# Kernel tuning notes

Hardware: AMD Instinct MI355X
Metric: run time of the kernel (lower is better)

The kernel has to match this reference:

```python
import jax, jax.numpy as jnp
import numpy as np

LEVELS = [(64, 64), (32, 32), (16, 16), (8, 8)]  # (H, W) per feature level
B, C, NH, NL, NP, NLAYERS, FFN = 8, 256, 8, 4, 4, 6, 1024
Q = sum(h * w for h, w in LEVELS)  # 5440
DH = C // NH


def setup_inputs() -> dict:
    key = jax.random.key(0)
    ks = iter(jax.random.split(key, 40))
    def rn(shape, s=0.02):
        return jax.random.normal(next(ks), shape, dtype=jnp.float32) * s
    return {
        'src_flat': jax.random.normal(next(ks), (B, Q, C), dtype=jnp.float32),
        'pos_flat': jax.random.normal(next(ks), (B, Q, C), dtype=jnp.float32) * 0.1,
        'level_embed': rn((NL, C), 0.1),
        'W_samp': rn((NLAYERS, C, NH * NL * NP * 2)),
        'b_samp': rn((NLAYERS, NH * NL * NP * 2), 0.1),
        'W_attn': rn((NLAYERS, C, NH * NL * NP)),
        'b_attn': rn((NLAYERS, NH * NL * NP), 0.1),
        'W_val': rn((NLAYERS, C, C)),
        'b_val': jnp.zeros((NLAYERS, C), jnp.float32),
        'W_out': rn((NLAYERS, C, C)),
        'b_out': jnp.zeros((NLAYERS, C), jnp.float32),
        'g1': jnp.ones((NLAYERS, C), jnp.float32),
        'b1': jnp.zeros((NLAYERS, C), jnp.float32),
        'W_fc1': rn((NLAYERS, C, FFN)),
        'b_fc1': jnp.zeros((NLAYERS, FFN), jnp.float32),
        'W_fc2': rn((NLAYERS, FFN, C)),
        'b_fc2': jnp.zeros((NLAYERS, C), jnp.float32),
        'g2': jnp.ones((NLAYERS, C), jnp.float32),
        'b2': jnp.zeros((NLAYERS, C), jnp.float32),
    }


def layer_norm(x, g, b):
    m = x.mean(-1, keepdims=True)
    v = ((x - m) ** 2).mean(-1, keepdims=True)
    return (x - m) * jax.lax.rsqrt(v + 1e-5) * g + b


def get_reference_points():
    # valid_ratios are all ones (masks are all-False), so ref pts are identical per level dim
    pts = []
    for (h, w) in LEVELS:
        ry = (jnp.arange(h, dtype=jnp.float32) + 0.5) / h
        rx = (jnp.arange(w, dtype=jnp.float32) + 0.5) / w
        yy, xx = jnp.meshgrid(ry, rx, indexing='ij')
        pts.append(jnp.stack([xx.ravel(), yy.ravel()], -1))
    return jnp.concatenate(pts, 0)  # [Q, 2] in (x, y)


def ms_deform_attn(query, src, ref_pts, Ws, bs, Wa, ba, Wv, bv, Wo, bo):
    value = (src @ Wv + bv).reshape(B, Q, NH, DH)
    off = (query @ Ws + bs).reshape(B, Q, NH, NL, NP, 2)
    aw = jax.nn.softmax((query @ Wa + ba).reshape(B, Q, NH, NL * NP), axis=-1)
    aw = aw.reshape(B, Q, NH, NL, NP).transpose(0, 2, 1, 3, 4)  # [B,NH,Q,NL,NP]
    normalizer = jnp.array([[w, h] for (h, w) in LEVELS], jnp.float32)  # (x, y) per level
    loc = ref_pts[None, :, None, None, None, :] + off / normalizer[None, None, None, :, None, :]
    out = jnp.zeros((B, NH, Q, DH), jnp.float32)
    start = 0
    for l, (h, w) in enumerate(LEVELS):
        v_l = value[:, start:start + h * w].transpose(0, 2, 1, 3)  # [B,NH,HW,DH]
        start += h * w
        loc_l = loc[:, :, :, l]  # [B,Q,NH,NP,2]
        x = loc_l[..., 0] * w - 0.5  # grid_sample align_corners=False pixel coords
        y = loc_l[..., 1] * h - 0.5
        x0 = jnp.floor(x)
        y0 = jnp.floor(y)
        fx = x - x0
        fy = y - y0
        sampled = jnp.zeros((B, NH, Q, NP, DH), jnp.float32)
        for dy, dx in ((0, 0), (0, 1), (1, 0), (1, 1)):
            cy = y0 + dy
            cx = x0 + dx
            wgt = (fy if dy else 1.0 - fy) * (fx if dx else 1.0 - fx)
            valid = (cy >= 0) & (cy < h) & (cx >= 0) & (cx < w)  # zero padding
            wgt = jnp.where(valid, wgt, 0.0)
            idx = (jnp.clip(cy, 0, h - 1) * w + jnp.clip(cx, 0, w - 1)).astype(jnp.int32)
            idx = idx.transpose(0, 2, 1, 3).reshape(B, NH, Q * NP)
            g = jnp.take_along_axis(v_l, idx[..., None], axis=2).reshape(B, NH, Q, NP, DH)
            sampled = sampled + g * wgt.transpose(0, 2, 1, 3)[..., None]
        out = out + (sampled * aw[:, :, :, l, :, None]).sum(3)
    out = out.transpose(0, 2, 1, 3).reshape(B, Q, C)
    return out @ Wo + bo


def reference(src_flat, pos_flat, level_embed, W_samp, b_samp, W_attn, b_attn, W_val, b_val, W_out, b_out, g1, b1, W_fc1, b_fc1, W_fc2, b_fc2, g2, b2):
    counts = np.array([h * w for h, w in LEVELS])
    lvl_emb = jnp.repeat(level_embed, counts, axis=0, total_repeat_length=Q)  # [Q,C]
    pos = pos_flat + lvl_emb[None]
    ref = get_reference_points()
    out = src_flat
    for i in range(NLAYERS):
        q = out + pos
        attn = ms_deform_attn(q, out, ref, W_samp[i], b_samp[i], W_attn[i], b_attn[i], W_val[i], b_val[i], W_out[i], b_out[i])
        out = layer_norm(out + attn, g1[i], b1[i])
        hid = jax.nn.relu(out @ W_fc1[i] + b_fc1[i]) @ W_fc2[i] + b_fc2[i]
        out = layer_norm(out + hid, g2[i], b2[i])
    return out
```

## Files before the change

### kernel.cpp

```cpp
#include <hip/hip_runtime.h>
#include <hip/hip_bf16.h>

#define NB 8
#define NC 256
#define NH_ 8
#define NLAYERS_ 6
#define FFN_ 1024
#define Q_ 5440
#define DH_ 32
#define M_ (NB*Q_)
#define MCH (M_/4)

typedef __attribute__((ext_vector_type(8))) short bf16x8;
typedef __attribute__((ext_vector_type(4))) short bf16x4;
typedef __attribute__((ext_vector_type(4))) float f32x4;
typedef __attribute__((ext_vector_type(4))) int i32x4;
typedef __attribute__((ext_vector_type(4))) unsigned int u32x4;
typedef unsigned int u32;

__device__ __forceinline__ unsigned short f2bf(float f) {
  unsigned int u = __float_as_uint(f);
  u += 0x7fffu + ((u >> 16) & 1u);
  return (unsigned short)(u >> 16);
}
__device__ __forceinline__ float bf2f(unsigned short s) {
  return __uint_as_float(((unsigned int)s) << 16);
}
__device__ __forceinline__ void gl16(const unsigned short* g, unsigned short* l) {
  __builtin_amdgcn_global_load_lds((const __attribute__((address_space(1))) u32*)(g),
                                   (__attribute__((address_space(3))) u32*)(l), 16, 0, 0);
}

__global__ void transpose_w2_k(const float* __restrict__ W, unsigned short* __restrict__ Wt,
                               int L, int Kd, int Nd, int NdTot, int nOff) {
  size_t total = (size_t)L * Nd * Kd;
  for (size_t i = (size_t)blockIdx.x * blockDim.x + threadIdx.x; i < total;
       i += (size_t)gridDim.x * blockDim.x) {
    int k = (int)(i % Kd);
    size_t r = i / Kd;
    int n = (int)(r % Nd);
    int l = (int)(r / Nd);
    Wt[((size_t)l * NdTot + nOff + n) * Kd + k] = f2bf(W[((size_t)l * Kd + k) * Nd + n]);
  }
}

__global__ void bias_cat_k(const float* __restrict__ bs, const float* __restrict__ ba,
                           float* __restrict__ bsa) {
  int i = blockIdx.x * blockDim.x + threadIdx.x;
  if (i >= NLAYERS_ * 384) return;
  int l = i / 384, n = i % 384;
  bsa[i] = (n < 256) ? bs[l * 256 + n] : ba[l * 128 + (n - 256)];
}

__global__ __launch_bounds__(256)
void pre_k(const float* __restrict__ src, const float* __restrict__ pf,
           const float* __restrict__ le, unsigned short* __restrict__ xb,
           unsigned short* __restrict__ pe, unsigned short* __restrict__ qb) {
  int row = blockIdx.x * 4 + (threadIdx.x >> 6);
  int lane = threadIdx.x & 63;
  size_t base = (size_t)row * NC + lane * 4;
  int q = row % Q_;
  int lvl = q < 4096 ? 0 : (q < 5120 ? 1 : (q < 5376 ? 2 : 3));
  f32x4 xv = *(const f32x4*)(src + base);
  f32x4 pv = *(const f32x4*)(pf + base) + *(const f32x4*)(le + lvl * NC + lane * 4);
  f32x4 qv = xv + pv;
  bf16x4 xo, po, qo;
#pragma unroll
  for (int j = 0; j < 4; ++j) {
    xo[j] = (short)f2bf(xv[j]); po[j] = (short)f2bf(pv[j]); qo[j] = (short)f2bf(qv[j]);
  }
  *(bf16x4*)(xb + base) = xo;
  *(bf16x4*)(pe + base) = po;
  *(bf16x4*)(qb + base) = qo;
}

__device__ __forceinline__ int swz(int r, int sl) { return sl ^ (r & 3) ^ ((r >> 2) & 3); }

template <bool RELU>
__global__ __launch_bounds__(256)
void gemm_k(const unsigned short* __restrict__ X, const unsigned short* __restrict__ Wt,
            const float* __restrict__ bias, unsigned short* __restrict__ Y,
            int Kdim, int Ndim) {
  __shared__ unsigned short Alds[2][128 * 32];
  __shared__ unsigned short Blds[2][128 * 32];
  const int t = threadIdx.x;
  const int n0 = blockIdx.x * 128;
  const int m0 = blockIdx.y * 128;
  const int wave = t >> 6, lane = t & 63;
  const int wr = wave >> 1, wc = wave & 1;
  const int lr = lane & 15, lk = lane >> 4;
  const int r0 = t >> 2, sl0 = t & 3;
  const int r1 = (256 + t) >> 2;
  const int gs0 = swz(r0, sl0);
  const int gs1 = swz(r1, sl0);
  const unsigned short* xp0 = X + (size_t)(m0 + r0) * Kdim + gs0 * 8;
  const unsigned short* wp0 = Wt + (size_t)(n0 + r0) * Kdim + gs0 * 8;
  const unsigned short* xp1 = X + (size_t)(m0 + r1) * Kdim + gs1 * 8;
  const unsigned short* wp1 = Wt + (size_t)(n0 + r1) * Kdim + gs1 * 8;

  f32x4 acc[4][4];
#pragma unroll
  for (int i = 0; i < 4; ++i)
#pragma unroll
    for (int j = 0; j < 4; ++j)
#pragma unroll
      for (int e = 0; e < 4; ++e) acc[i][j][e] = 0.f;

  auto stage = [&](int buf, int kt) {
    gl16(xp0 + kt, Alds[buf] + t * 8);
    gl16(wp0 + kt, Blds[buf] + t * 8);
    gl16(xp1 + kt, Alds[buf] + (256 + t) * 8);
    gl16(wp1 + kt, Blds[buf] + (256 + t) * 8);
  };

  stage(0, 0);
  __syncthreads();
  const int nt = Kdim >> 5;
  int cur = 0;
  for (int ti = 0; ti < nt; ++ti) {
    if (ti + 1 < nt) stage(cur ^ 1, (ti + 1) << 5);
    bf16x8 ar[4], br[4];
#pragma unroll
    for (int fi = 0; fi < 4; ++fi) {
      int r = wr * 64 + fi * 16 + lr;
      ar[fi] = *(const bf16x8*)&Alds[cur][r * 32 + swz(r, lk) * 8];
    }
#pragma unroll
    for (int fj = 0; fj < 4; ++fj) {
      int r = wc * 64 + fj * 16 + lr;
      br[fj] = *(const bf16x8*)&Blds[cur][r * 32 + swz(r, lk) * 8];
    }
#pragma unroll
    for (int fi = 0; fi < 4; ++fi)
#pragma unroll
      for (int fj = 0; fj < 4; ++fj)
        acc[fi][fj] = __builtin_amdgcn_mfma_f32_16x16x32_bf16(ar[fi], br[fj], acc[fi][fj], 0, 0, 0);
    __syncthreads();
    cur ^= 1;
  }

  const int orow = m0 + wr * 64;
  const int ocol = n0 + wc * 64;
#pragma unroll
  for (int fi = 0; fi < 4; ++fi)
#pragma unroll
    for (int fj = 0; fj < 4; ++fj) {
      int col = ocol + fj * 16 + lr;
      float bv = bias[col];
#pragma unroll
      for (int rr = 0; rr < 4; ++rr) {
        int row = orow + fi * 16 + lk * 4 + rr;
        float v = acc[fi][fj][rr] + bv;
        if constexpr (RELU) v = fmaxf(v, 0.f);
        Y[(size_t)row * Ndim + col] = f2bf(v);
      }
    }
}

__global__ __launch_bounds__(256)
void samp_k(const unsigned short* __restrict__ value, const unsigned short* __restrict__ sa,
            unsigned short* __restrict__ attn_feat) {
  __shared__ float lw[4][128][4];
  __shared__ int   la[4][128][4];
  const int wid = threadIdx.x >> 6, lane = threadIdx.x & 63;
  const int bq = blockIdx.x * 4 + wid;
  const int q = bq % Q_;
  const int b = bq / Q_;

  int lvl = q < 4096 ? 0 : (q < 5120 ? 1 : (q < 5376 ? 2 : 3));
  int qrem = q - (lvl == 0 ? 0 : lvl == 1 ? 4096 : lvl == 2 ? 5120 : 5376);
  int wlog = 6 - lvl;
  float inv = __uint_as_float((unsigned)(127 - wlog) << 23);
  float refx = ((qrem & ((1 << wlog) - 1)) + 0.5f) * inv;
  float refy = ((qrem >> wlog) + 0.5f) * inv;
  const unsigned short* sa_bq = sa + (size_t)bq * 384;

  const int h_s = lane >> 3;
  const int s0 = (lane & 7) * 2;
  unsigned lg01 = *(const unsigned*)&sa_bq[256 + h_s * 16 + s0];
  float lg0 = bf2f((unsigned short)(lg01 & 0xffff));
  float lg1 = bf2f((unsigned short)(lg01 >> 16));
  float mx = fmaxf(lg0, lg1);
  mx = fmaxf(mx, __shfl_xor(mx, 1));
  mx = fmaxf(mx, __shfl_xor(mx, 2));
  mx = fmaxf(mx, __shfl_xor(mx, 4));
  float e0 = __expf(lg0 - mx), e1 = __expf(lg1 - mx);
  float sm = e0 + e1;
  sm += __shfl_xor(sm, 1);
  sm += __shfl_xor(sm, 2);
  sm += __shfl_xor(sm, 4);
  float rs = 1.0f / sm;

#pragma unroll
  for (int j = 0; j < 2; ++j) {
    int s = s0 + j;
    float aw = (j ? e1 : e0) * rs;
    unsigned oxy = *(const unsigned*)&sa_bq[h_s * 32 + s * 2];
    float ox = bf2f((unsigned short)(oxy & 0xffff));
    float oy = bf2f((unsigned short)(oxy >> 16));
    int sl = s >> 2;
    int swl = 6 - sl;
    int sw = 1 << swl;
    int sstart = (sl == 0) ? 0 : (sl == 1) ? 4096 : (sl == 2) ? 5120 : 5376;
    float x = fmaf(refx, (float)sw, ox) - 0.5f;
    float y = fmaf(refy, (float)sw, oy) - 0.5f;
    float x0f = floorf(x), y0f = floorf(y);
    float fx = x - x0f, fy = y - y0f;
    int x0 = (int)x0f, y0 = (int)y0f;
    int rowbase = b * Q_ + sstart;
    f32x4 wv; i32x4 av;
#pragma unroll
    for (int c = 0; c < 4; ++c) {
      int dy = c >> 1, dx = c & 1;
      int cy = y0 + dy, cx = x0 + dx;
      float wgt = (dy ? fy : 1.f - fy) * (dx ? fx : 1.f - fx);
      bool valid = (cy >= 0) & (cy < sw) & (cx >= 0) & (cx < sw);
      wgt = valid ? wgt : 0.f;
      int ccy = min(max(cy, 0), sw - 1);
      int ccx = min(max(cx, 0), sw - 1);
      wv[c] = wgt * aw;
      av[c] = ((rowbase + (ccy << swl) + ccx) * NH_ + h_s) * DH_;
    }
    int idx = s * 8 + (h_s ^ (s & 7));
    *(f32x4*)&lw[wid][idx][0] = wv;
    *(i32x4*)&la[wid][idx][0] = av;
  }
  __syncthreads();

  const int h = lane >> 3;
  const int half = (lane >> 2) & 1;
  const int quad = lane & 3;
  const unsigned short* vq = value + quad * 8;
  f32x4 accA = {0.f, 0.f, 0.f, 0.f}, accB = {0.f, 0.f, 0.f, 0.f};
#pragma unroll
  for (int i = 0; i < 8; ++i) {
    int s = half * 8 + i;
    int idx = s * 8 + (h ^ (s & 7));
    f32x4 wv = *(const f32x4*)&lw[wid][idx][0];
    i32x4 av = *(const i32x4*)&la[wid][idx][0];
#pragma unroll
    for (int c = 0; c < 4; ++c) {
      u32x4 g = *(const u32x4*)(vq + av[c]);
      f32x4 v0, v1;
      v0[0] = __uint_as_float(g[0] << 16); v0[1] = __uint_as_float(g[0] & 0xffff0000u);
      v0[2] = __uint_as_float(g[1] << 16); v0[3] = __uint_as_float(g[1] & 0xffff0000u);
      v1[0] = __uint_as_float(g[2] << 16); v1[1] = __uint_as_float(g[2] & 0xffff0000u);
      v1[2] = __uint_as_float(g[3] << 16); v1[3] = __uint_as_float(g[3] & 0xffff0000u);
      float wcc = wv[c];
      accA += v0 * wcc;
      accB += v1 * wcc;
    }
  }
#pragma unroll
  for (int j = 0; j < 4; ++j) {
    accA[j] += __shfl_xor(accA[j], 4);
    accB[j] += __shfl_xor(accB[j], 4);
  }
  if (half == 0) {
    bf16x8 ov;
    ov[0] = (short)f2bf(accA[0]); ov[1] = (short)f2bf(accA[1]);
    ov[2] = (short)f2bf(accA[2]); ov[3] = (short)f2bf(accA[3]);
    ov[4] = (short)f2bf(accB[0]); ov[5] = (short)f2bf(accB[1]);
    ov[6] = (short)f2bf(accB[2]); ov[7] = (short)f2bf(accB[3]);
    *(bf16x8*)(attn_feat + (size_t)bq * NC + h * DH_ + quad * 8) = ov;
  }
}

__device__ __forceinline__ f32x4 ln_core(f32x4 xv, const float* g, const float* bta, int lane) {
  float ssum = xv[0] + xv[1] + xv[2] + xv[3];
#pragma unroll
  for (int o = 1; o <= 32; o <<= 1) ssum += __shfl_xor(ssum, o);
  float mean = ssum * (1.0f / NC);
  f32x4 cv = xv - mean;
  float s2 = cv[0] * cv[0] + cv[1] * cv[1] + cv[2] * cv[2] + cv[3] * cv[3];
#pragma unroll
  for (int o = 1; o <= 32; o <<= 1) s2 += __shfl_xor(s2, o);
  float rstd = rsqrtf(s2 * (1.0f / NC) + 1e-5f);
  f32x4 gv = *(const f32x4*)(g + lane * 4);
  f32x4 bv = *(const f32x4*)(bta + lane * 4);
  return cv * rstd * gv + bv;
}
__device__ __forceinline__ f32x4 ldbf4(const unsigned short* p) {
  bf16x4 v = *(const bf16x4*)p;
  f32x4 r;
#pragma unroll
  for (int j = 0; j < 4; ++j) r[j] = bf2f((unsigned short)v[j]);
  return r;
}
__device__ __forceinline__ void stbf4(unsigned short* p, f32x4 v) {
  bf16x4 o;
#pragma unroll
  for (int j = 0; j < 4; ++j) o[j] = (short)f2bf(v[j]);
  *(bf16x4*)p = o;
}

__global__ __launch_bounds__(256)
void ln_mid_k(const unsigned short* __restrict__ xb, const unsigned short* __restrict__ delta,
              const float* __restrict__ g, const float* __restrict__ bta,
              unsigned short* __restrict__ xm) {
  int row = blockIdx.x * 4 + (threadIdx.x >> 6);
  int lane = threadIdx.x & 63;
  size_t base = (size_t)row * NC + lane * 4;
  f32x4 xv = ldbf4(xb + base) + ldbf4(delta + base);
  f32x4 ov = ln_core(xv, g, bta, lane);
  stbf4(xm + base, ov);
}

template <bool FINAL>
__global__ __launch_bounds__(256)
void ln_end_k(const unsigned short* __restrict__ xm, const unsigned short* __restrict__ delta,
              const float* __restrict__ g, const float* __restrict__ bta,
              const unsigned short* __restrict__ pe,
              unsigned short* __restrict__ xb, unsigned short* __restrict__ qb,
              float* __restrict__ outf) {
  int row = blockIdx.x * 4 + (threadIdx.x >> 6);
  int lane = threadIdx.x & 63;
  size_t base = (size_t)row * NC + lane * 4;
  f32x4 xv = ldbf4(xm + base) + ldbf4(delta + base);
  f32x4 ov = ln_core(xv, g, bta, lane);
  stbf4(xb + base, ov);
  f32x4 qv = ov + ldbf4(pe + base);
  stbf4(qb + base, qv);
  if constexpr (FINAL) *(f32x4*)(outf + base) = ov;
}

extern "C" void kernel_launch(void* const* d_in, const int* in_sizes, int n_in,
                              void* d_out, int out_size, void* d_ws, size_t ws_size,
                              hipStream_t stream) {
  const float* src      = (const float*)d_in[0];
  const float* pos_flat = (const float*)d_in[1];
  const float* lvl_emb  = (const float*)d_in[2];
  const float* W_samp   = (const float*)d_in[3];
  const float* b_samp   = (const float*)d_in[4];
  const float* W_attn   = (const float*)d_in[5];
  const float* b_attn   = (const float*)d_in[6];
  const float* W_val    = (const float*)d_in[7];
  const float* b_val    = (const float*)d_in[8];
  const float* W_out    = (const float*)d_in[9];
  const float* b_out    = (const float*)d_in[10];
  const float* g1       = (const float*)d_in[11];
  const float* b1       = (const float*)d_in[12];
  const float* W_fc1    = (const float*)d_in[13];
  const float* b_fc1    = (const float*)d_in[14];
  const float* W_fc2    = (const float*)d_in[15];
  const float* b_fc2    = (const float*)d_in[16];
  const float* g2       = (const float*)d_in[17];
  const float* b2       = (const float*)d_in[18];

  char* ws = (char*)d_ws;
  size_t o = 0;
  auto alloc = [&](size_t bytes) {
    void* p = ws + o;
    o += (bytes + 255) & ~(size_t)255;
    return p;
  };
  unsigned short* bb    = (unsigned short*)alloc((size_t)M_ * NC * 2);
  unsigned short* sa    = (unsigned short*)alloc((size_t)M_ * 384 * 2);
  unsigned short* af    = (unsigned short*)alloc((size_t)M_ * NC * 2);
  unsigned short* xb    = (unsigned short*)alloc((size_t)M_ * NC * 2);
  unsigned short* xm    = (unsigned short*)alloc((size_t)M_ * NC * 2);
  unsigned short* qb    = (unsigned short*)alloc((size_t)M_ * NC * 2);
  unsigned short* pe    = (unsigned short*)alloc((size_t)M_ * NC * 2);
  unsigned short* Wv_t  = (unsigned short*)alloc((size_t)6 * 256 * 256 * 2);
  unsigned short* Wsa_t = (unsigned short*)alloc((size_t)6 * 384 * 256 * 2);
  unsigned short* Wo_t  = (unsigned short*)alloc((size_t)6 * 256 * 256 * 2);
  unsigned short* Wf1_t = (unsigned short*)alloc((size_t)6 * 1024 * 256 * 2);
  unsigned short* Wf2_t = (unsigned short*)alloc((size_t)6 * 256 * 1024 * 2);
  float* bsa            = (float*)alloc((size_t)6 * 384 * 4);

  transpose_w2_k<<<1536, 256, 0, stream>>>(W_val, Wv_t, 6, 256, 256, 256, 0);
  transpose_w2_k<<<1536, 256, 0, stream>>>(W_samp, Wsa_t, 6, 256, 256, 384, 0);
  transpose_w2_k<<<768, 256, 0, stream>>>(W_attn, Wsa_t, 6, 256, 128, 384, 256);
  transpose_w2_k<<<1536, 256, 0, stream>>>(W_out, Wo_t, 6, 256, 256, 256, 0);
  transpose_w2_k<<<3072, 256, 0, stream>>>(W_fc1, Wf1_t, 6, 256, 1024, 1024, 0);
  transpose_w2_k<<<3072, 256, 0, stream>>>(W_fc2, Wf2_t, 6, 1024, 256, 256, 0);
  bias_cat_k<<<9, 256, 0, stream>>>(b_samp, b_attn, bsa);
  pre_k<<<M_ / 4, 256, 0, stream>>>(src, pos_flat, lvl_emb, xb, pe, qb);

  for (int i = 0; i < NLAYERS_; ++i) {
    gemm_k<false><<<dim3(2, M_ / 128), 256, 0, stream>>>(
        xb, Wv_t + (size_t)i * 65536, b_val + i * 256, bb, 256, 256);
    gemm_k<false><<<dim3(3, M_ / 128), 256, 0, stream>>>(
        qb, Wsa_t + (size_t)i * 98304, bsa + i * 384, sa, 256, 384);
    samp_k<<<M_ / 4, 256, 0, stream>>>(bb, sa, af);
    gemm_k<false><<<dim3(2, M_ / 128), 256, 0, stream>>>(
        af, Wo_t + (size_t)i * 65536, b_out + i * 256, sa, 256, 256);
    ln_mid_k<<<M_ / 4, 256, 0, stream>>>(xb, sa, g1 + i * 256, b1 + i * 256, xm);
    for (int c = 0; c < 4; ++c) {
      gemm_k<true><<<dim3(8, MCH / 128), 256, 0, stream>>>(
          xm + (size_t)c * MCH * NC, Wf1_t + (size_t)i * 262144, b_fc1 + i * 1024, bb, 256, 1024);
      gemm_k<false><<<dim3(2, MCH / 128), 256, 0, stream>>>(
          bb, Wf2_t + (size_t)i * 262144, b_fc2 + i * 256, sa + (size_t)c * MCH * NC, 1024, 256);
    }
    if (i == NLAYERS_ - 1)
      ln_end_k<true><<<M_ / 4, 256, 0, stream>>>(xm, sa, g2 + i * 256, b2 + i * 256,
                                                 pe, xb, qb, (float*)d_out);
    else
      ln_end_k<false><<<M_ / 4, 256, 0, stream>>>(xm, sa, g2 + i * 256, b2 + i * 256,
                                                  pe, xb, qb, nullptr);
  }
}
```

Before: 1.811 ms.

## Stage GEMM epilogue through LDS, fuse value/sampling GEMMs, halve FFN chunking

The GEMM epilogue now writes the bf16 tile into padded shared memory and then copies whole rows out to global memory with 16-byte vector stores, replacing the scattered 2-byte stores. The value projection and the sampling/attention projection are merged into one launch that picks its weights by blockIdx.x, which cuts launch count and gives a larger grid. The FFN is processed in two row chunks instead of four, so the intermediate buffer grows but there are fewer launches. Shared memory per block rises to 128*136 bf16 (about 34 KB), which may lower occupancy.

After: 1.698 ms. 1.07x faster.

```diff
diff --git a/kernel.cpp b/kernel.cpp
--- a/kernel.cpp
+++ b/kernel.cpp
@@ -9,7 +9,7 @@
 #define Q_ 5440
 #define DH_ 32
 #define M_ (NB*Q_)
-#define MCH (M_/4)
+#define MC2 (M_/2)
 
 typedef __attribute__((ext_vector_type(8))) short bf16x8;
 typedef __attribute__((ext_vector_type(4))) short bf16x4;
@@ -17,6 +17,7 @@
 typedef __attribute__((ext_vector_type(4))) int i32x4;
 typedef __attribute__((ext_vector_type(4))) unsigned int u32x4;
 typedef unsigned int u32;
+typedef unsigned short ushort_t;
 
 __device__ __forceinline__ unsigned short f2bf(float f) {
   unsigned int u = __float_as_uint(f);
@@ -75,17 +76,16 @@
 }
 
 __device__ __forceinline__ int swz(int r, int sl) { return sl ^ (r & 3) ^ ((r >> 2) & 3); }
+#define ES 136
 
 template <bool RELU>
-__global__ __launch_bounds__(256)
-void gemm_k(const unsigned short* __restrict__ X, const unsigned short* __restrict__ Wt,
-            const float* __restrict__ bias, unsigned short* __restrict__ Y,
-            int Kdim, int Ndim) {
-  __shared__ unsigned short Alds[2][128 * 32];
-  __shared__ unsigned short Blds[2][128 * 32];
+__device__ __forceinline__ void gemm_body(const unsigned short* X, const unsigned short* Wt,
+                                          const float* bias, unsigned short* Y,
+                                          int Kdim, int Ndim, int n0, int m0,
+                                          unsigned short* SH) {
+  unsigned short* A0 = SH;
+  unsigned short* B0 = SH + 8192;
   const int t = threadIdx.x;
-  const int n0 = blockIdx.x * 128;
-  const int m0 = blockIdx.y * 128;
   const int wave = t >> 6, lane = t & 63;
   const int wr = wave >> 1, wc = wave & 1;
   const int lr = lane & 15, lk = lane >> 4;
@@ -107,10 +107,10 @@
       for (int e = 0; e < 4; ++e) acc[i][j][e] = 0.f;
 
   auto stage = [&](int buf, int kt) {
-    gl16(xp0 + kt, Alds[buf] + t * 8);
-    gl16(wp0 + kt, Blds[buf] + t * 8);
-    gl16(xp1 + kt, Alds[buf] + (256 + t) * 8);
-    gl16(wp1 + kt, Blds[buf] + (256 + t) * 8);
+    gl16(xp0 + kt, A0 + buf * 4096 + t * 8);
+    gl16(wp0 + kt, B0 + buf * 4096 + t * 8);
+    gl16(xp1 + kt, A0 + buf * 4096 + (256 + t) * 8);
+    gl16(wp1 + kt, B0 + buf * 4096 + (256 + t) * 8);
   };
 
   stage(0, 0);
@@ -123,12 +123,12 @@
 #pragma unroll
     for (int fi = 0; fi < 4; ++fi) {
       int r = wr * 64 + fi * 16 + lr;
-      ar[fi] = *(const bf16x8*)&Alds[cur][r * 32 + swz(r, lk) * 8];
+      ar[fi] = *(const bf16x8*)&A0[cur * 4096 + r * 32 + swz(r, lk) * 8];
     }
 #pragma unroll
     for (int fj = 0; fj < 4; ++fj) {
       int r = wc * 64 + fj * 16 + lr;
-      br[fj] = *(const bf16x8*)&Blds[cur][r * 32 + swz(r, lk) * 8];
+      br[fj] = *(const bf16x8*)&B0[cur * 4096 + r * 32 + swz(r, lk) * 8];
     }
 #pragma unroll
     for (int fi = 0; fi < 4; ++fi)
@@ -139,22 +139,51 @@
     cur ^= 1;
   }
 
-  const int orow = m0 + wr * 64;
-  const int ocol = n0 + wc * 64;
 #pragma unroll
   for (int fi = 0; fi < 4; ++fi)
 #pragma unroll
     for (int fj = 0; fj < 4; ++fj) {
-      int col = ocol + fj * 16 + lr;
-      float bv = bias[col];
+      int col = wc * 64 + fj * 16 + lr;
+      float bv = bias[n0 + col];
 #pragma unroll
       for (int rr = 0; rr < 4; ++rr) {
-        int row = orow + fi * 16 + lk * 4 + rr;
+        int row = wr * 64 + fi * 16 + lk * 4 + rr;
         float v = acc[fi][fj][rr] + bv;
         if constexpr (RELU) v = fmaxf(v, 0.f);
-        Y[(size_t)row * Ndim + col] = f2bf(v);
+        SH[row * ES + col] = f2bf(v);
       }
     }
+  __syncthreads();
+  {
+    int row = t >> 1, hcol = (t & 1) * 64;
+    const unsigned short* sp = SH + row * ES + hcol;
+    unsigned short* dp = Y + (size_t)(m0 + row) * Ndim + n0 + hcol;
+#pragma unroll
+    for (int j = 0; j < 8; ++j)
+      *(bf16x8*)(dp + j * 8) = *(const bf16x8*)(sp + j * 8);
+  }
+}
+
+template <bool RELU>
+__global__ __launch_bounds__(256)
+void gemm_k(const unsigned short* __restrict__ X, const unsigned short* __restrict__ Wt,
+            const float* __restrict__ bias, unsigned short* __restrict__ Y,
+            int Kdim, int Ndim) {
+  __shared__ unsigned short SH[128 * ES];
+  gemm_body<RELU>(X, Wt, bias, Y, Kdim, Ndim, blockIdx.x * 128, blockIdx.y * 128, SH);
+}
+
+__global__ __launch_bounds__(256)
+void gemm_vs_k(const unsigned short* __restrict__ X0, const unsigned short* __restrict__ W0,
+               const float* __restrict__ b0, unsigned short* __restrict__ Y0,
+               const unsigned short* __restrict__ X1, const unsigned short* __restrict__ W1,
+               const float* __restrict__ b1, unsigned short* __restrict__ Y1) {
+  __shared__ unsigned short SH[128 * ES];
+  int bx = blockIdx.x, m0 = blockIdx.y * 128;
+  if (bx < 2)
+    gemm_body<false>(X0, W0, b0, Y0, 256, 256, bx * 128, m0, SH);
+  else
+    gemm_body<false>(X1, W1, b1, Y1, 256, 384, (bx - 2) * 128, m0, SH);
 }
 
 __global__ __launch_bounds__(256)
@@ -354,7 +383,7 @@
     o += (bytes + 255) & ~(size_t)255;
     return p;
   };
-  unsigned short* bb    = (unsigned short*)alloc((size_t)M_ * NC * 2);
+  unsigned short* bb    = (unsigned short*)alloc((size_t)MC2 * FFN_ * 2);
   unsigned short* sa    = (unsigned short*)alloc((size_t)M_ * 384 * 2);
   unsigned short* af    = (unsigned short*)alloc((size_t)M_ * NC * 2);
   unsigned short* xb    = (unsigned short*)alloc((size_t)M_ * NC * 2);
@@ -378,19 +407,18 @@
   pre_k<<<M_ / 4, 256, 0, stream>>>(src, pos_flat, lvl_emb, xb, pe, qb);
 
   for (int i = 0; i < NLAYERS_; ++i) {
-    gemm_k<false><<<dim3(2, M_ / 128), 256, 0, stream>>>(
-        xb, Wv_t + (size_t)i * 65536, b_val + i * 256, bb, 256, 256);
-    gemm_k<false><<<dim3(3, M_ / 128), 256, 0, stream>>>(
-        qb, Wsa_t + (size_t)i * 98304, bsa + i * 384, sa, 256, 384);
+    gemm_vs_k<<<dim3(5, M_ / 128), 256, 0, stream>>>(
+        xb, Wv_t + (size_t)i * 65536, b_val + i * 256, bb,
+        qb, Wsa_t + (size_t)i * 98304, bsa + i * 384, sa);
     samp_k<<<M_ / 4, 256, 0, stream>>>(bb, sa, af);
     gemm_k<false><<<dim3(2, M_ / 128), 256, 0, stream>>>(
         af, Wo_t + (size_t)i * 65536, b_out + i * 256, sa, 256, 256);
     ln_mid_k<<<M_ / 4, 256, 0, stream>>>(xb, sa, g1 + i * 256, b1 + i * 256, xm);
-    for (int c = 0; c < 4; ++c) {
-      gemm_k<true><<<dim3(8, MCH / 128), 256, 0, stream>>>(
-          xm + (size_t)c * MCH * NC, Wf1_t + (size_t)i * 262144, b_fc1 + i * 1024, bb, 256, 1024);
-      gemm_k<false><<<dim3(2, MCH / 128), 256, 0, stream>>>(
-          bb, Wf2_t + (size_t)i * 262144, b_fc2 + i * 256, sa + (size_t)c * MCH * NC, 1024, 256);
+    for (int c = 0; c < 2; ++c) {
+      gemm_k<true><<<dim3(8, MC2 / 128), 256, 0, stream>>>(
+          xm + (size_t)c * MC2 * NC, Wf1_t + (size_t)i * 262144, b_fc1 + i * 1024, bb, 256, 1024);
+      gemm_k<false><<<dim3(2, MC2 / 128), 256, 0, stream>>>(
+          bb, Wf2_t + (size_t)i * 262144, b_fc2 + i * 256, sa + (size_t)c * MC2 * NC, 1024, 256);
     }
     if (i == NLAYERS_ - 1)
       ln_end_k<true><<<M_ / 4, 256, 0, stream>>>(xm, sa, g2 + i * 256, b2 + i * 256,
```
